# Performance work log

Hardware: AMD Instinct MI355X
Metric: run time of the kernel (lower is better)

## Reference

```python
import jax, jax.numpy as jnp
import numpy as np

NQ = 6       # total qubits
NF = 4
NL = 2       # layers
B = 65536    # batch
WEIGHT_INIT_STD = 0.01


def _apply_1q(state, gate, w):
    """Apply a 2x2 gate (shared (2,2) or per-sample (B,2,2)) to qubit w.
    state: (B, 2,2,2,2,2,2) complex64, axis w+1 is qubit w (PennyLane wire order)."""
    ax = w + 1
    s = jnp.moveaxis(state, ax, -1)
    shp = s.shape
    s = s.reshape(shp[0], -1, 2)
    if gate.ndim == 2:
        s = jnp.einsum('ij,bkj->bki', gate, s)
    else:
        s = jnp.einsum('bij,bkj->bki', gate, s)
    return jnp.moveaxis(s.reshape(shp), -1, ax)


def _cnot(state, c, t):
    """CNOT with control c, target t: flip target axis where control bit = 1."""
    ac, at = c + 1, t + 1
    s0 = jax.lax.index_in_dim(state, 0, ac, keepdims=True)
    s1 = jnp.flip(jax.lax.index_in_dim(state, 1, ac, keepdims=True), axis=at)
    return jnp.concatenate([s0, s1], axis=ac)


def _ry(theta):
    ct = jnp.cos(theta * 0.5)
    st = jnp.sin(theta * 0.5)
    return jnp.stack([jnp.stack([ct, -st]), jnp.stack([st, ct])]).astype(jnp.complex64)


def _circuit(x, weights, ancilla_bias):
    b = x.shape[0]
    state = jnp.zeros((b,) + (2,) * NQ, jnp.complex64)
    state = state.at[(slice(None),) + (0,) * NQ].set(1.0)  # |000000>
    # RX(x[:, w]) encoding on qubits 0..3 (batched gates)
    half = x.astype(jnp.float32) * 0.5
    c = jnp.cos(half).astype(jnp.complex64)
    s = (-1j) * jnp.sin(half).astype(jnp.complex64)
    for w in range(NF):
        g = jnp.stack([jnp.stack([c[:, w], s[:, w]], -1),
                       jnp.stack([s[:, w], c[:, w]], -1)], -2)  # (B,2,2)
        state = _apply_1q(state, g, w)
    # RY ancilla init on qubits 4, 5
    state = _apply_1q(state, _ry(ancilla_bias[0]), 4)
    state = _apply_1q(state, _ry(ancilla_bias[1]), 5)
    # entangling layers: CNOT ring then RY rotations
    for l in range(weights.shape[0]):
        for w in range(NQ):
            state = _cnot(state, w, (w + 1) % NQ)
        for w in range(NQ):
            state = _apply_1q(state, _ry(weights[l, w]), w)
    # <Z_w> for w in 0..3
    p = state.real ** 2 + state.imag ** 2  # (B,2,...,2)
    outs = []
    for w in range(NF):
        pw = p.sum(axis=tuple(a for a in range(1, NQ + 1) if a != w + 1))  # (B,2)
        outs.append(pw[:, 0] - pw[:, 1])
    return jnp.stack(outs, -1).astype(jnp.float32)  # (B, 4)


def setup_inputs() -> dict:
    key = jax.random.key(0)
    k1, k2 = jax.random.split(key)
    x = jax.random.normal(k1, (B, NF), jnp.float32)
    weights = jax.random.normal(k2, (NL, NQ), jnp.float32) * WEIGHT_INIT_STD
    ancilla_bias = jnp.zeros((2,), jnp.float32)
    return {"x": x, "weights": weights, "ancilla_bias": ancilla_bias}


def reference(x, weights, ancilla_bias):
    return _circuit(x, weights, ancilla_bias)
```

## Files before the change

### kernel.cpp

```cpp
#include <hip/hip_runtime.h>


#define NL 2

__global__ __launch_bounds__(256) void qcirc6_l4_kernel(
    const float* __restrict__ x,
    const float* __restrict__ weights,
    const float* __restrict__ bias,
    float* __restrict__ out,
    int B)
{
    const int gid = blockIdx.x * blockDim.x + threadIdx.x;
    const int sample = gid >> 2;
    if (sample >= B) return;
    const int lane = threadIdx.x & 63;
    const int sub = lane & 3;

    const float4 xv = reinterpret_cast<const float4*>(x)[sample];
    const float xs[4] = {xv.x, xv.y, xv.z, xv.w};

    float re[16], im[16];
    #pragma unroll
    for (int t = 0; t < 16; ++t) { re[t] = 0.0f; im[t] = 0.0f; }
    re[0] = (sub == 0) ? 1.0f : 0.0f;

    #pragma unroll
    for (int w = 0; w < 4; ++w) {
        float s, c;
        __sincosf(xs[w] * 0.5f, &s, &c);
        const int m = 1 << (3 - w);
        #pragma unroll
        for (int t = 0; t < 16; ++t) {
            if (t & m) continue;
            const int j = t | m;
            const float a0r = re[t], a0i = im[t];
            const float a1r = re[j], a1i = im[j];
            re[t] =  c * a0r + s * a1i;
            im[t] =  c * a0i - s * a1r;
            re[j] =  s * a0i + c * a1r;
            im[j] = -s * a0r + c * a1i;
        }
    }

    auto ry_lane = [&](float st, float ct, int lmask) {
        const float sg = (sub & lmask) ? st : -st;
        #pragma unroll
        for (int t = 0; t < 16; ++t) {
            const float pr = __shfl_xor(re[t], lmask, 64);
            const float pi = __shfl_xor(im[t], lmask, 64);
            re[t] = ct * re[t] + sg * pr;
            im[t] = ct * im[t] + sg * pi;
        }
    };

    auto ry_local = [&](float st, float ct, int m) {
        #pragma unroll
        for (int t = 0; t < 16; ++t) {
            if (t & m) continue;
            const int j = t | m;
            const float a0r = re[t], a0i = im[t];
            const float a1r = re[j], a1i = im[j];
            re[t] = ct * a0r - st * a1r;
            im[t] = ct * a0i - st * a1i;
            re[j] = st * a0r + ct * a1r;
            im[j] = st * a0i + ct * a1i;
        }
    };

    auto cnot_local = [&](int cm, int tm) {
        #pragma unroll
        for (int t = 0; t < 16; ++t) {
            if ((t & cm) && !(t & tm)) {
                const int j = t | tm;
                float tmp;
                tmp = re[t]; re[t] = re[j]; re[j] = tmp;
                tmp = im[t]; im[t] = im[j]; im[j] = tmp;
            }
        }
    };

    {
        float st, ct;
        __sincosf(bias[0] * 0.5f, &st, &ct);
        ry_lane(st, ct, 2);
        __sincosf(bias[1] * 0.5f, &st, &ct);
        ry_lane(st, ct, 1);
    }

    const int perm45 = (sub & 2) ? (lane ^ 1) : lane;
    const bool c50 = (sub & 1) != 0;

    #pragma unroll
    for (int l = 0; l < NL; ++l) {
        cnot_local(8, 4);
        cnot_local(4, 2);
        cnot_local(2, 1);
        #pragma unroll
        for (int t = 1; t < 16; t += 2) {
            re[t] = __shfl_xor(re[t], 2, 64);
            im[t] = __shfl_xor(im[t], 2, 64);
        }
        #pragma unroll
        for (int t = 0; t < 16; ++t) {
            re[t] = __shfl(re[t], perm45, 64);
            im[t] = __shfl(im[t], perm45, 64);
        }
        #pragma unroll
        for (int t = 0; t < 8; ++t) {
            const int j = t | 8;
            float a, b;
            a = re[t]; b = re[j];
            re[t] = c50 ? b : a;  re[j] = c50 ? a : b;
            a = im[t]; b = im[j];
            im[t] = c50 ? b : a;  im[j] = c50 ? a : b;
        }
        float st, ct;
        __sincosf(weights[l * 6 + 0] * 0.5f, &st, &ct); ry_local(st, ct, 8);
        __sincosf(weights[l * 6 + 1] * 0.5f, &st, &ct); ry_local(st, ct, 4);
        __sincosf(weights[l * 6 + 2] * 0.5f, &st, &ct); ry_local(st, ct, 2);
        __sincosf(weights[l * 6 + 3] * 0.5f, &st, &ct); ry_local(st, ct, 1);
        __sincosf(weights[l * 6 + 4] * 0.5f, &st, &ct); ry_lane(st, ct, 2);
        __sincosf(weights[l * 6 + 5] * 0.5f, &st, &ct); ry_lane(st, ct, 1);
    }

    float z0 = 0.f, z1 = 0.f, z2 = 0.f, z3 = 0.f;
    #pragma unroll
    for (int t = 0; t < 16; ++t) {
        const float p = re[t] * re[t] + im[t] * im[t];
        z0 += (t & 8) ? -p : p;
        z1 += (t & 4) ? -p : p;
        z2 += (t & 2) ? -p : p;
        z3 += (t & 1) ? -p : p;
    }
    z0 += __shfl_xor(z0, 1, 64); z0 += __shfl_xor(z0, 2, 64);
    z1 += __shfl_xor(z1, 1, 64); z1 += __shfl_xor(z1, 2, 64);
    z2 += __shfl_xor(z2, 1, 64); z2 += __shfl_xor(z2, 2, 64);
    z3 += __shfl_xor(z3, 1, 64); z3 += __shfl_xor(z3, 2, 64);

    const float zsel = (sub == 0) ? z0 : (sub == 1) ? z1 : (sub == 2) ? z2 : z3;
    out[sample * 4 + sub] = zsel;
}

extern "C" void kernel_launch(void* const* d_in, const int* in_sizes, int n_in,
                              void* d_out, int out_size, void* d_ws, size_t ws_size,
                              hipStream_t stream) {
    const float* x       = (const float*)d_in[0];
    const float* weights = (const float*)d_in[1];
    const float* bias    = (const float*)d_in[2];
    float* out = (float*)d_out;
    const int B = in_sizes[0] / 4;
    const int threads = B * 4;
    qcirc6_l4_kernel<<<(threads + 255) / 256, 256, 0, stream>>>(x, weights, bias, out, B);
}
```

Before: 72.43 us.

## Use DPP quad permutes, analytic product-state init, and packed float2 math

Swaps ds_bpermute-based shuffles for DPP quad permutes, both for the lane-level RY gates and for the CNOT lane permutations and reductions. The RX encoding and ancilla RY steps are replaced by a closed-form product-state amplitude per lane, with the needed phases. The CNOT(5,0) swap is folded into the following RY on qubit 0 through lane-dependent coefficients, and complex amplitudes are held as float2 vectors so packed FMA can be used. Each lane now loads one x element and the broadcasts go through DPP. These changes cut instruction count and LDS-permute latency, but they depend on exact DPP control encodings and on the quad layout.

```diff
diff --git a/kernel.cpp b/kernel.cpp
--- a/kernel.cpp
+++ b/kernel.cpp
@@ -3,7 +3,28 @@
 
 #define NL 2
 
-__global__ __launch_bounds__(256) void qcirc6_l4_kernel(
+typedef float v2f __attribute__((ext_vector_type(2)));
+
+template<int CTRL>
+__device__ __forceinline__ float dppf(float v) {
+    return __int_as_float(__builtin_amdgcn_update_dpp(
+        0, __float_as_int(v), CTRL, 0xF, 0xF, true));
+}
+template<int CTRL>
+__device__ __forceinline__ v2f dpp2(v2f v) {
+    v2f r; r.x = dppf<CTRL>(v.x); r.y = dppf<CTRL>(v.y); return r;
+}
+__device__ __forceinline__ v2f splat(float f) { v2f r; r.x = f; r.y = f; return r; }
+
+#define QP_XOR1  0xB1
+#define QP_XOR2  0x4E
+#define QP_C45   0xB4
+#define QP_BC0   0x00
+#define QP_BC1   0x55
+#define QP_BC2   0xAA
+#define QP_BC3   0xFF
+
+__global__ __launch_bounds__(256) void qcirc6_dpp_kernel(
     const float* __restrict__ x,
     const float* __restrict__ weights,
     const float* __restrict__ bias,
@@ -13,132 +34,122 @@
     const int gid = blockIdx.x * blockDim.x + threadIdx.x;
     const int sample = gid >> 2;
     if (sample >= B) return;
-    const int lane = threadIdx.x & 63;
-    const int sub = lane & 3;
+    const int sub = gid & 3;
 
-    const float4 xv = reinterpret_cast<const float4*>(x)[sample];
-    const float xs[4] = {xv.x, xv.y, xv.z, xv.w};
+    float sh, ch;
+    __sincosf(x[gid] * 0.5f, &sh, &ch);
+    const float c0 = dppf<QP_BC0>(ch), s0 = dppf<QP_BC0>(sh);
+    const float c1 = dppf<QP_BC1>(ch), s1 = dppf<QP_BC1>(sh);
+    const float c2 = dppf<QP_BC2>(ch), s2 = dppf<QP_BC2>(sh);
+    const float c3 = dppf<QP_BC3>(ch), s3 = dppf<QP_BC3>(sh);
 
-    float re[16], im[16];
+    float sb0, cb0, sb1, cb1;
+    __sincosf(bias[0] * 0.5f, &sb0, &cb0);
+    __sincosf(bias[1] * 0.5f, &sb1, &cb1);
+    const float laneF = ((sub & 2) ? sb0 : cb0) * ((sub & 1) ? sb1 : cb1);
+
+    const float v01[4] = {c0 * c1, c0 * s1, s0 * c1, s0 * s1};
+    const float v23[4] = {c2 * c3, c2 * s3, s2 * c3, s2 * s3};
+
+    v2f a[16];
     #pragma unroll
-    for (int t = 0; t < 16; ++t) { re[t] = 0.0f; im[t] = 0.0f; }
-    re[0] = (sub == 0) ? 1.0f : 0.0f;
-
-    #pragma unroll
-    for (int w = 0; w < 4; ++w) {
-        float s, c;
-        __sincosf(xs[w] * 0.5f, &s, &c);
-        const int m = 1 << (3 - w);
-        #pragma unroll
-        for (int t = 0; t < 16; ++t) {
-            if (t & m) continue;
-            const int j = t | m;
-            const float a0r = re[t], a0i = im[t];
-            const float a1r = re[j], a1i = im[j];
-            re[t] =  c * a0r + s * a1i;
-            im[t] =  c * a0i - s * a1r;
-            re[j] =  s * a0i + c * a1r;
-            im[j] = -s * a0r + c * a1i;
-        }
+    for (int t = 0; t < 16; ++t) {
+        const float v = laneF * v01[t >> 2] * v23[t & 3];
+        const int m = ((t & 1) + ((t >> 1) & 1) + ((t >> 2) & 1) + ((t >> 3) & 1)) & 3;
+        v2f av;
+        if      (m == 0) { av.x =  v;   av.y = 0.f; }
+        else if (m == 1) { av.x = 0.f;  av.y = -v;  }
+        else if (m == 2) { av.x = -v;   av.y = 0.f; }
+        else             { av.x = 0.f;  av.y =  v;  }
+        a[t] = av;
     }
 
-    auto ry_lane = [&](float st, float ct, int lmask) {
-        const float sg = (sub & lmask) ? st : -st;
-        #pragma unroll
-        for (int t = 0; t < 16; ++t) {
-            const float pr = __shfl_xor(re[t], lmask, 64);
-            const float pi = __shfl_xor(im[t], lmask, 64);
-            re[t] = ct * re[t] + sg * pr;
-            im[t] = ct * im[t] + sg * pi;
-        }
-    };
-
-    auto ry_local = [&](float st, float ct, int m) {
-        #pragma unroll
-        for (int t = 0; t < 16; ++t) {
-            if (t & m) continue;
-            const int j = t | m;
-            const float a0r = re[t], a0i = im[t];
-            const float a1r = re[j], a1i = im[j];
-            re[t] = ct * a0r - st * a1r;
-            im[t] = ct * a0i - st * a1i;
-            re[j] = st * a0r + ct * a1r;
-            im[j] = st * a0i + ct * a1i;
-        }
-    };
-
-    auto cnot_local = [&](int cm, int tm) {
-        #pragma unroll
-        for (int t = 0; t < 16; ++t) {
-            if ((t & cm) && !(t & tm)) {
-                const int j = t | tm;
-                float tmp;
-                tmp = re[t]; re[t] = re[j]; re[j] = tmp;
-                tmp = im[t]; im[t] = im[j]; im[j] = tmp;
-            }
-        }
-    };
-
-    {
-        float st, ct;
-        __sincosf(bias[0] * 0.5f, &st, &ct);
-        ry_lane(st, ct, 2);
-        __sincosf(bias[1] * 0.5f, &st, &ct);
-        ry_lane(st, ct, 1);
-    }
-
-    const int perm45 = (sub & 2) ? (lane ^ 1) : lane;
     const bool c50 = (sub & 1) != 0;
 
     #pragma unroll
     for (int l = 0; l < NL; ++l) {
-        cnot_local(8, 4);
-        cnot_local(4, 2);
-        cnot_local(2, 1);
         #pragma unroll
-        for (int t = 1; t < 16; t += 2) {
-            re[t] = __shfl_xor(re[t], 2, 64);
-            im[t] = __shfl_xor(im[t], 2, 64);
+        for (int pass = 0; pass < 3; ++pass) {
+            const int cm = 8 >> pass, tm = 4 >> pass;
+            #pragma unroll
+            for (int t = 0; t < 16; ++t) {
+                if ((t & cm) && !(t & tm)) {
+                    const int j = t | tm;
+                    v2f tmp = a[t]; a[t] = a[j]; a[j] = tmp;
+                }
+            }
         }
         #pragma unroll
-        for (int t = 0; t < 16; ++t) {
-            re[t] = __shfl(re[t], perm45, 64);
-            im[t] = __shfl(im[t], perm45, 64);
+        for (int t = 1; t < 16; t += 2) a[t] = dpp2<QP_XOR2>(a[t]);
+        #pragma unroll
+        for (int t = 0; t < 16; ++t) a[t] = dpp2<QP_C45>(a[t]);
+
+        float st, ct;
+        __sincosf(weights[l * 6 + 0] * 0.5f, &st, &ct);
+        {
+            const v2f al = splat(c50 ? -st : ct);
+            const v2f be = splat(c50 ?  ct : -st);
+            const v2f ga = splat(c50 ?  ct : st);
+            const v2f de = splat(c50 ?  st : ct);
+            #pragma unroll
+            for (int t = 0; t < 8; ++t) {
+                const int j = t | 8;
+                const v2f a0 = a[t], a1 = a[j];
+                a[t] = al * a0 + be * a1;
+                a[j] = ga * a0 + de * a1;
+            }
         }
         #pragma unroll
-        for (int t = 0; t < 8; ++t) {
-            const int j = t | 8;
-            float a, b;
-            a = re[t]; b = re[j];
-            re[t] = c50 ? b : a;  re[j] = c50 ? a : b;
-            a = im[t]; b = im[j];
-            im[t] = c50 ? b : a;  im[j] = c50 ? a : b;
+        for (int w = 1; w < 4; ++w) {
+            __sincosf(weights[l * 6 + w] * 0.5f, &st, &ct);
+            const v2f ctv = splat(ct), stv = splat(st);
+            const int m = 8 >> w;
+            #pragma unroll
+            for (int t = 0; t < 16; ++t) {
+                if (t & m) continue;
+                const int j = t | m;
+                const v2f a0 = a[t], a1 = a[j];
+                a[t] = ctv * a0 - stv * a1;
+                a[j] = stv * a0 + ctv * a1;
+            }
         }
-        float st, ct;
-        __sincosf(weights[l * 6 + 0] * 0.5f, &st, &ct); ry_local(st, ct, 8);
-        __sincosf(weights[l * 6 + 1] * 0.5f, &st, &ct); ry_local(st, ct, 4);
-        __sincosf(weights[l * 6 + 2] * 0.5f, &st, &ct); ry_local(st, ct, 2);
-        __sincosf(weights[l * 6 + 3] * 0.5f, &st, &ct); ry_local(st, ct, 1);
-        __sincosf(weights[l * 6 + 4] * 0.5f, &st, &ct); ry_lane(st, ct, 2);
-        __sincosf(weights[l * 6 + 5] * 0.5f, &st, &ct); ry_lane(st, ct, 1);
+        __sincosf(weights[l * 6 + 4] * 0.5f, &st, &ct);
+        {
+            const v2f ctv = splat(ct), sgv = splat((sub & 2) ? st : -st);
+            #pragma unroll
+            for (int t = 0; t < 16; ++t) {
+                const v2f p = dpp2<QP_XOR2>(a[t]);
+                a[t] = ctv * a[t] + sgv * p;
+            }
+        }
+        __sincosf(weights[l * 6 + 5] * 0.5f, &st, &ct);
+        {
+            const v2f ctv = splat(ct), sgv = splat((sub & 1) ? st : -st);
+            #pragma unroll
+            for (int t = 0; t < 16; ++t) {
+                const v2f p = dpp2<QP_XOR1>(a[t]);
+                a[t] = ctv * a[t] + sgv * p;
+            }
+        }
     }
 
     float z0 = 0.f, z1 = 0.f, z2 = 0.f, z3 = 0.f;
     #pragma unroll
     for (int t = 0; t < 16; ++t) {
-        const float p = re[t] * re[t] + im[t] * im[t];
+        const v2f sq = a[t] * a[t];
+        const float p = sq.x + sq.y;
         z0 += (t & 8) ? -p : p;
         z1 += (t & 4) ? -p : p;
         z2 += (t & 2) ? -p : p;
         z3 += (t & 1) ? -p : p;
     }
-    z0 += __shfl_xor(z0, 1, 64); z0 += __shfl_xor(z0, 2, 64);
-    z1 += __shfl_xor(z1, 1, 64); z1 += __shfl_xor(z1, 2, 64);
-    z2 += __shfl_xor(z2, 1, 64); z2 += __shfl_xor(z2, 2, 64);
-    z3 += __shfl_xor(z3, 1, 64); z3 += __shfl_xor(z3, 2, 64);
+    z0 += dppf<QP_XOR1>(z0); z0 += dppf<QP_XOR2>(z0);
+    z1 += dppf<QP_XOR1>(z1); z1 += dppf<QP_XOR2>(z1);
+    z2 += dppf<QP_XOR1>(z2); z2 += dppf<QP_XOR2>(z2);
+    z3 += dppf<QP_XOR1>(z3); z3 += dppf<QP_XOR2>(z3);
 
     const float zsel = (sub == 0) ? z0 : (sub == 1) ? z1 : (sub == 2) ? z2 : z3;
-    out[sample * 4 + sub] = zsel;
+    out[gid] = zsel;
 }
 
 extern "C" void kernel_launch(void* const* d_in, const int* in_sizes, int n_in,
@@ -150,5 +161,5 @@
     float* out = (float*)d_out;
     const int B = in_sizes[0] / 4;
     const int threads = B * 4;
-    qcirc6_l4_kernel<<<(threads + 255) / 256, 256, 0, stream>>>(x, weights, bias, out, B);
+    qcirc6_dpp_kernel<<<(threads + 255) / 256, 256, 0, stream>>>(x, weights, bias, out, B);
 }
```

Measured after the change: 63.59 us. -12.2%, faster.
